# Kernel tuning notes

Measured on AMD Instinct MI355X. Metric: run time of the kernel, lower is better.

The kernel has to match this reference:

```python
import jax, jax.numpy as jnp
import numpy as np

N_LEVELS = 16
F = 2
LOG2_T = 19
T = 1 << LOG2_T
BASE_RES = 16.0
FINEST_RES = 512.0
N_SAMPLES = 128
NEAR, FAR = 2.0, 6.0
BOX_MIN = jnp.array([-1.5, -1.5, -1.5], jnp.float32)
BOX_MAX = jnp.array([1.5, 1.5, 1.5], jnp.float32)
GEO_FEAT = 15
OUT_CH = 4

_PRIMES = np.array([1, 2654435761, 805459861], dtype=np.uint32)
_OFFSETS = np.array([[i, j, k] for i in (0, 1) for j in (0, 1) for k in (0, 1)], dtype=np.int32)  # [8,3]
_B = np.exp((np.log(FINEST_RES) - np.log(BASE_RES)) / (N_LEVELS - 1))
_RESOLUTIONS = np.floor(BASE_RES * _B ** np.arange(N_LEVELS)).astype(np.float32)


def setup_inputs() -> dict:
    key = jax.random.key(0)
    ks = jax.random.split(key, 10)
    n_rays = 16384
    o = jax.random.uniform(ks[0], (n_rays, 3), jnp.float32, -0.5, 0.5)
    d = jax.random.normal(ks[1], (n_rays, 3), jnp.float32)
    d = d / jnp.linalg.norm(d, axis=-1, keepdims=True)
    rays = jnp.concatenate([o, d], -1)
    hash_tables = jax.random.uniform(ks[2], (N_LEVELS, T, F), jnp.float32, -1e-4, 1e-4)
    def w(k, di, do):
        return jax.random.normal(k, (di, do), jnp.float32) * (1.0 / np.sqrt(di))
    return dict(
        rays=rays,
        hash_tables=hash_tables,
        ws0=w(ks[3], 32, 64), ws1=w(ks[4], 64, 64), ws2=w(ks[5], 64, 1 + GEO_FEAT),
        wc0=w(ks[6], 16 + GEO_FEAT, 64), wc1=w(ks[7], 64, 64), wc2=w(ks[8], 64, 64), wc3=w(ks[9], 64, OUT_CH - 1),
    )


def _hash_embed(x, tables):
    """Multi-res hash grid: x [P,3] world coords, tables [L,T,F] -> ([P,L*F], keep_mask [P])."""
    xc = jnp.clip(x, BOX_MIN, BOX_MAX)
    keep = jnp.all(x == xc, axis=-1)
    offs = jnp.asarray(_OFFSETS)          # [8,3]
    primes = jnp.asarray(_PRIMES)         # uint32
    feats = []
    for l in range(N_LEVELS):
        grid = (BOX_MAX - BOX_MIN) / _RESOLUTIONS[l]
        bl = jnp.floor((xc - BOX_MIN) / grid).astype(jnp.int32)   # [P,3] bottom-left voxel index
        vmin = bl.astype(jnp.float32) * grid + BOX_MIN
        wts = (xc - vmin) / grid                                  # trilinear weights [P,3]
        corners = (bl[:, None, :] + offs[None]).astype(jnp.uint32)  # [P,8,3]
        h = (corners[..., 0] * primes[0]) ^ (corners[..., 1] * primes[1]) ^ (corners[..., 2] * primes[2])
        idx = (h & jnp.uint32(T - 1)).astype(jnp.int32)           # [P,8]
        e = tables[l][idx]                                        # [P,8,F]
        w0, w1, w2 = wts[:, 0:1], wts[:, 1:2], wts[:, 2:3]
        c00 = e[:, 0] * (1 - w0) + e[:, 4] * w0
        c01 = e[:, 1] * (1 - w0) + e[:, 5] * w0
        c10 = e[:, 2] * (1 - w0) + e[:, 6] * w0
        c11 = e[:, 3] * (1 - w0) + e[:, 7] * w0
        c0 = c00 * (1 - w1) + c10 * w1
        c1 = c01 * (1 - w1) + c11 * w1
        feats.append(c0 * (1 - w2) + c1 * w2)
    return jnp.concatenate(feats, -1), keep


def _sh_encode(d):
    """Degree-4 spherical harmonics encoding, [P,3] -> [P,16]."""
    x, y, z = d[..., 0], d[..., 1], d[..., 2]
    xx, yy, zz = x * x, y * y, z * z
    xy, yz, xz = x * y, y * z, x * z
    C0 = 0.28209479177387814
    C1 = 0.4886025119029199
    C2 = (1.0925484305920792, -1.0925484305920792, 0.31539156525252005, -1.0925484305920792, 0.5462742152960396)
    C3 = (-0.5900435899266435, 2.890611442640554, -0.4570457994644658, 0.3731763325901154,
          -0.4570457994644658, 1.445305721320277, -0.5900435899266435)
    return jnp.stack([
        jnp.full_like(x, C0),
        -C1 * y, C1 * z, -C1 * x,
        C2[0] * xy, C2[1] * yz, C2[2] * (2.0 * zz - xx - yy), C2[3] * xz, C2[4] * (xx - yy),
        C3[0] * y * (3.0 * xx - yy), C3[1] * xy * z, C3[2] * y * (4.0 * zz - xx - yy),
        C3[3] * z * (2.0 * zz - 3.0 * xx - 3.0 * yy), C3[4] * x * (4.0 * zz - xx - yy),
        C3[5] * z * (xx - yy), C3[6] * x * (xx - 3.0 * yy),
    ], axis=-1)


def _forward(rays, hash_tables, ws0, ws1, ws2, wc0, wc1, wc2, wc3):
    n_rays = rays.shape[0]
    o, d = rays[:, :3], rays[:, 3:6]
    z = jnp.linspace(NEAR, FAR, N_SAMPLES, dtype=jnp.float32)
    zvals = jnp.broadcast_to(z, (n_rays, N_SAMPLES))
    pts = o[:, None, :] + d[:, None, :] * z[None, :, None]       # [N,S,3]
    P = n_rays * N_SAMPLES
    pts_f = pts.reshape(P, 3)
    dirs_f = jnp.broadcast_to(d[:, None, :], (n_rays, N_SAMPLES, 3)).reshape(P, 3)

    enc_pts, keep = _hash_embed(pts_f, hash_tables)              # [P,32], [P]
    enc_dirs = _sh_encode(dirs_f)                                # [P,16]

    # NeRFSmall: bias-free sigma net then color net
    h = jnp.maximum(enc_pts @ ws0, 0.0)
    h = jnp.maximum(h @ ws1, 0.0)
    h = h @ ws2                                                   # [P, 1+GEO_FEAT]
    sigma, geo = h[:, 0], h[:, 1:]
    hc = jnp.concatenate([enc_dirs, geo], -1)
    hc = jnp.maximum(hc @ wc0, 0.0)
    hc = jnp.maximum(hc @ wc1, 0.0)
    hc = jnp.maximum(hc @ wc2, 0.0)
    color = hc @ wc3                                              # [P, OUT_CH-1]

    sigma = jnp.where(keep, sigma, 0.0)                           # output[~keep_mask, -1] = 0
    raw = jnp.concatenate([color, sigma[:, None]], -1).reshape(n_rays, N_SAMPLES, OUT_CH)

    # Integrator (raw2outputs)
    dists = zvals[:, 1:] - zvals[:, :-1]
    dists = jnp.concatenate([dists, jnp.full((n_rays, 1), 1e10, jnp.float32)], -1)
    dists = dists * jnp.linalg.norm(d, axis=-1, keepdims=True)
    chs = jax.nn.sigmoid(raw[..., :-1])
    alpha = 1.0 - jnp.exp(-jnp.maximum(raw[..., -1], 0.0) * dists)
    trans = jnp.cumprod(1.0 - alpha + 1e-10, axis=-1)
    trans = jnp.concatenate([jnp.ones((n_rays, 1), jnp.float32), trans[:, :-1]], -1)
    weights = alpha * trans
    chs_map = jnp.einsum('ns,nsc->nc', weights, chs)
    depth_map = jnp.sum(weights * zvals, -1)
    probs = jnp.concatenate([weights, 1.0 - jnp.sum(weights, -1, keepdims=True) + 1e-6], -1)
    p = probs / jnp.sum(probs, -1, keepdims=True)
    sparsity_loss = -jnp.sum(p * jnp.log(jnp.clip(p, 1e-37)), -1)
    return chs_map, depth_map, sparsity_loss


def reference(rays, hash_tables, ws0, ws1, ws2, wc0, wc1, wc2, wc3):
    return _forward(rays, hash_tables, ws0, ws1, ws2, wc0, wc1, wc2, wc3)
```

## Files before the change

### kernel.cpp

```cpp
#include <hip/hip_runtime.h>

#define NRAYS 16384
#define NLEV  16
#define THASH 524288
#define MAXACT 48
#define MAXPTS (NRAYS*MAXACT)
#define MBLK  512
#define MGRID 1024

__device__ __forceinline__ float zval32(int i) {
  const float step = 4.0f / 127.0f;
  return __fadd_rn(2.0f, __fmul_rn((float)i, step));
}
__device__ __forceinline__ float pcoord(float o, float d, float z) {
  return __fadd_rn(o, __fmul_rn(d, z));
}

__global__ __launch_bounds__(64)
void k_classify(const float* __restrict__ rays,
                float* __restrict__ sh,
                unsigned* __restrict__ rn) {
  int r = blockIdx.x * 64 + threadIdx.x;
  if (r >= NRAYS) return;
  float ox = rays[6*r+0], oy = rays[6*r+1], oz = rays[6*r+2];
  float dx = rays[6*r+3], dy = rays[6*r+4], dz = rays[6*r+5];
  float x = dx, y = dy, z = dz;
  float xx = x*x, yy = y*y, zz = z*z, xy = x*y, yz = y*z, xz = x*z;
  float* shp = sh + 16*r;
  shp[0]  = 0.28209479177387814f;
  shp[1]  = -0.4886025119029199f * y;
  shp[2]  =  0.4886025119029199f * z;
  shp[3]  = -0.4886025119029199f * x;
  shp[4]  =  1.0925484305920792f * xy;
  shp[5]  = -1.0925484305920792f * yz;
  shp[6]  =  0.31539156525252005f * (2.0f*zz - xx - yy);
  shp[7]  = -1.0925484305920792f * xz;
  shp[8]  =  0.5462742152960396f * (xx - yy);
  shp[9]  = -0.5900435899266435f * y * (3.0f*xx - yy);
  shp[10] =  2.890611442640554f  * xy * z;
  shp[11] = -0.4570457994644658f * y * (4.0f*zz - xx - yy);
  shp[12] =  0.3731763325901154f * z * (2.0f*zz - 3.0f*xx - 3.0f*yy);
  shp[13] = -0.4570457994644658f * x * (4.0f*zz - xx - yy);
  shp[14] =  1.445305721320277f  * z * (xx - yy);
  shp[15] = -0.5900435899266435f * x * (xx - 3.0f*yy);
  int n = 0;
  for (int i = 0; i < 128; ++i) {
    float zi = zval32(i);
    float px = pcoord(ox, dx, zi);
    float py = pcoord(oy, dy, zi);
    float pz = pcoord(oz, dz, zi);
    bool in = (px >= -1.5f) && (px <= 1.5f) && (py >= -1.5f) && (py <= 1.5f)
           && (pz >= -1.5f) && (pz <= 1.5f);
    if (!in) break;
    ++n;
  }
  rn[r] = (unsigned)n;
}

__global__ __launch_bounds__(1024)
void k_scan(const unsigned* __restrict__ rn,
            unsigned* __restrict__ rbase,
            unsigned* __restrict__ counter,
            unsigned* __restrict__ plist) {
  __shared__ unsigned wsum[16];
  const int t = threadIdx.x;
  const int lane = t & 63, wid = t >> 6;
  unsigned nv[16];
  const uint4* rn4 = (const uint4*)rn;
  unsigned tot = 0;
#pragma unroll
  for (int k = 0; k < 4; ++k) {
    uint4 a = rn4[t*4 + k];
    nv[4*k+0] = a.x; nv[4*k+1] = a.y; nv[4*k+2] = a.z; nv[4*k+3] = a.w;
    tot += a.x + a.y + a.z + a.w;
  }
  unsigned incl = tot;
#pragma unroll
  for (int off = 1; off < 64; off <<= 1) {
    unsigned v = __shfl_up(incl, off);
    if (lane >= off) incl += v;
  }
  if (lane == 63) wsum[wid] = incl;
  __syncthreads();
  if (t == 0) {
    unsigned acc = 0;
#pragma unroll
    for (int w = 0; w < 16; ++w) { unsigned x = wsum[w]; wsum[w] = acc; acc += x; }
    *counter = acc;
  }
  __syncthreads();
  unsigned base = wsum[wid] + (incl - tot);
#pragma unroll
  for (int j = 0; j < 16; ++j) {
    int r = t*16 + j;
    rbase[r] = base;
    unsigned nj = nv[j];
    for (unsigned i = 0; i < nj; ++i) plist[base + i] = (unsigned)(r*128) + i;
    base += nj;
  }
}

template<int IN, int TOTOUT, int JC, bool RELU>
__device__ __forceinline__ void layer(const float* __restrict__ W, int jbase,
                                      const float* __restrict__ in,
                                      float* __restrict__ out, int lane) {
  float acc[JC];
#pragma unroll
  for (int j = 0; j < JC; ++j) acc[j] = 0.0f;
#pragma unroll 4
  for (int k = 0; k < IN; ++k) {
    float a = in[k*64 + lane];
    const float* Wk = W + k*TOTOUT + jbase;
#pragma unroll
    for (int j = 0; j < JC; ++j) acc[j] = fmaf(a, Wk[j], acc[j]);
  }
#pragma unroll
  for (int j = 0; j < JC; ++j)
    out[(jbase + j)*64 + lane] = RELU ? fmaxf(acc[j], 0.0f) : acc[j];
}

__global__ __launch_bounds__(MBLK)
void k_mlp(const float* __restrict__ rays,
           const float* __restrict__ tables,
           const float* __restrict__ w_s0, const float* __restrict__ w_s1,
           const float* __restrict__ w_s2, const float* __restrict__ w_c0,
           const float* __restrict__ w_c1, const float* __restrict__ w_c2,
           const float* __restrict__ w_c3,
           const float* __restrict__ sh,
           const unsigned* __restrict__ counter,
           const unsigned* __restrict__ plist,
           float4* __restrict__ results) {
  __shared__ float bufA[64*64];
  __shared__ float bufB[64*64];
  __shared__ float sig_s[64];
  __shared__ unsigned pid_s[64];
  const int t = threadIdx.x;
  const int lane = t & 63;
  const int q = __builtin_amdgcn_readfirstlane(t >> 6);
  const unsigned count = *counter;
  const unsigned ntiles = (count + 63u) >> 6;
  const float RESF[NLEV] = {16.f,20.f,25.f,32.f,40.f,50.f,64.f,80.f,
                            101.f,128.f,161.f,203.f,256.f,322.f,406.f,512.f};
  for (unsigned tile = blockIdx.x; tile < ntiles; tile += MGRID) {
    unsigned s0 = tile << 6;
    if (t < 64) {
      unsigned s = s0 + (unsigned)t;
      pid_s[t] = (s < count) ? plist[s] : 0u;
    }
    __syncthreads();
    {
      unsigned pid = pid_s[lane];
      int r = (int)(pid >> 7);
      int i = (int)(pid & 127u);
      float zi = zval32(i);
      float px = pcoord(rays[6*r+0], rays[6*r+3], zi);
      float py = pcoord(rays[6*r+1], rays[6*r+4], zi);
      float pz = pcoord(rays[6*r+2], rays[6*r+5], zi);
      float xcx = fminf(fmaxf(px, -1.5f), 1.5f);
      float xcy = fminf(fmaxf(py, -1.5f), 1.5f);
      float xcz = fminf(fmaxf(pz, -1.5f), 1.5f);
#pragma unroll
      for (int li = 0; li < 2; ++li) {
        int l = 2*q + li;
        const float grid = 3.0f / RESF[l];
        float bfx = floorf(__fdiv_rn(__fadd_rn(xcx, 1.5f), grid));
        float bfy = floorf(__fdiv_rn(__fadd_rn(xcy, 1.5f), grid));
        float bfz = floorf(__fdiv_rn(__fadd_rn(xcz, 1.5f), grid));
        float vmx = __fadd_rn(__fmul_rn(bfx, grid), -1.5f);
        float vmy = __fadd_rn(__fmul_rn(bfy, grid), -1.5f);
        float vmz = __fadd_rn(__fmul_rn(bfz, grid), -1.5f);
        float wx = __fdiv_rn(__fsub_rn(xcx, vmx), grid);
        float wy = __fdiv_rn(__fsub_rn(xcy, vmy), grid);
        float wz = __fdiv_rn(__fsub_rn(xcz, vmz), grid);
        unsigned cx0 = (unsigned)(int)bfx, cy0 = (unsigned)(int)bfy, cz0 = (unsigned)(int)bfz;
        unsigned cx1 = cx0 + 1u, cy1 = cy0 + 1u, cz1 = cz0 + 1u;
        unsigned hy0 = cy0*2654435761u, hy1 = cy1*2654435761u;
        unsigned hz0 = cz0*805459861u,  hz1 = cz1*805459861u;
        const float2* tb = (const float2*)tables + (size_t)l*THASH;
        float2 e000 = tb[(cx0^hy0^hz0)&(THASH-1)];
        float2 e001 = tb[(cx0^hy0^hz1)&(THASH-1)];
        float2 e010 = tb[(cx0^hy1^hz0)&(THASH-1)];
        float2 e011 = tb[(cx0^hy1^hz1)&(THASH-1)];
        float2 e100 = tb[(cx1^hy0^hz0)&(THASH-1)];
        float2 e101 = tb[(cx1^hy0^hz1)&(THASH-1)];
        float2 e110 = tb[(cx1^hy1^hz0)&(THASH-1)];
        float2 e111 = tb[(cx1^hy1^hz1)&(THASH-1)];
        float iwx = 1.f-wx, iwy = 1.f-wy, iwz = 1.f-wz;
        float c00a = e000.x*iwx + e100.x*wx, c00b = e000.y*iwx + e100.y*wx;
        float c01a = e001.x*iwx + e101.x*wx, c01b = e001.y*iwx + e101.y*wx;
        float c10a = e010.x*iwx + e110.x*wx, c10b = e010.y*iwx + e110.y*wx;
        float c11a = e011.x*iwx + e111.x*wx, c11b = e011.y*iwx + e111.y*wx;
        float c0a = c00a*iwy + c10a*wy, c0b = c00b*iwy + c10b*wy;
        float c1a = c01a*iwy + c11a*wy, c1b = c01b*iwy + c11b*wy;
        bufA[(2*l+0)*64 + lane] = c0a*iwz + c1a*wz;
        bufA[(2*l+1)*64 + lane] = c0b*iwz + c1b*wz;
      }
    }
    __syncthreads();
    layer<32,64,8,true >(w_s0, q*8, bufA, bufB, lane); __syncthreads();
    layer<64,64,8,true >(w_s1, q*8, bufB, bufA, lane); __syncthreads();
    layer<64,16,2,false>(w_s2, q*2, bufA, bufB, lane); __syncthreads();
    if (q == 0) sig_s[lane] = bufB[0*64 + lane];
    for (int idx = t; idx < 31*64; idx += MBLK) {
      int k = idx >> 6, p = idx & 63;
      float v;
      if (k < 16) v = sh[(pid_s[p] >> 7)*16 + k];
      else        v = bufB[(k-15)*64 + p];
      bufA[idx] = v;
    }
    __syncthreads();
    layer<31,64,8,true >(w_c0, q*8, bufA, bufB, lane); __syncthreads();
    layer<64,64,8,true >(w_c1, q*8, bufB, bufA, lane); __syncthreads();
    layer<64,64,8,true >(w_c2, q*8, bufA, bufB, lane); __syncthreads();
    if (q < 3) layer<64,3,1,false>(w_c3, q, bufB, bufA, lane);
    __syncthreads();
    if (q == 0) {
      unsigned s = s0 + (unsigned)lane;
      if (s < count) {
        float4 res;
        res.x = sig_s[lane];
        res.y = bufA[0*64 + lane];
        res.z = bufA[1*64 + lane];
        res.w = bufA[2*64 + lane];
        results[s] = res;
      }
    }
    __syncthreads();
  }
}

__global__ __launch_bounds__(256)
void k_comp(const float* __restrict__ rays,
            const unsigned* __restrict__ rbase,
            const unsigned* __restrict__ rn,
            const float4* __restrict__ results,
            float* __restrict__ out) {
  __shared__ float s_al[4][64];
  __shared__ float s_c0[4][64];
  __shared__ float s_c1[4][64];
  __shared__ float s_c2[4][64];
  const int wid  = threadIdx.x >> 6;
  const int lane = threadIdx.x & 63;
  const int r = blockIdx.x * 4 + wid;
  float dx = rays[6*r+3], dy = rays[6*r+4], dz = rays[6*r+5];
  float dnorm = sqrtf(dx*dx + dy*dy + dz*dz);
  const int n = (int)rn[r];
  const unsigned base = rbase[r];
  const float step = 4.0f/127.0f;
  const float diststep = __fmul_rn(step, dnorm);
  if (lane < n) {
    float4 rs = results[base + lane];
    float sg = fmaxf(rs.x, 0.f);
    s_al[wid][lane] = -expm1f(-__fmul_rn(sg, diststep));
    s_c0[wid][lane] = 1.f/(1.f + expf(-rs.y));
    s_c1[wid][lane] = 1.f/(1.f + expf(-rs.z));
    s_c2[wid][lane] = 1.f/(1.f + expf(-rs.w));
  }
  __syncthreads();
  if (lane == 0) {
    float S = 0.f, ch0 = 0.f, ch1 = 0.f, ch2 = 0.f, dep = 0.f, trans = 1.f;
    for (int i = 0; i < n; ++i) {
      float alpha = s_al[wid][i];
      float w = __fmul_rn(alpha, trans);
      trans = __fmul_rn(trans, __fadd_rn(__fsub_rn(1.f, alpha), 1e-10f));
      S += w; ch0 += w*s_c0[wid][i]; ch1 += w*s_c1[wid][i]; ch2 += w*s_c2[wid][i];
      dep += w*zval32(i);
    }
    float rem  = __fadd_rn(__fsub_rn(1.f, S), 1e-6f);
    float Stot = __fadd_rn(S, rem);
    float loss = 0.f, trans2 = 1.f;
    for (int i = 0; i < n; ++i) {
      float alpha = s_al[wid][i];
      float w = __fmul_rn(alpha, trans2);
      trans2 = __fmul_rn(trans2, __fadd_rn(__fsub_rn(1.f, alpha), 1e-10f));
      float p = __fdiv_rn(w, Stot);
      loss += p * logf(fmaxf(p, 1e-37f));
    }
    float pl = __fdiv_rn(rem, Stot);
    loss += pl * logf(fmaxf(pl, 1e-37f));
    out[3*r+0] = ch0; out[3*r+1] = ch1; out[3*r+2] = ch2;
    out[3*NRAYS + r] = dep;
    out[4*NRAYS + r] = -loss;
  }
}

extern "C" void kernel_launch(void* const* d_in, const int* in_sizes, int n_in,
                              void* d_out, int out_size, void* d_ws, size_t ws_size,
                              hipStream_t stream) {
  const float* rays   = (const float*)d_in[0];
  const float* tables = (const float*)d_in[1];
  const float* ws0    = (const float*)d_in[2];
  const float* ws1    = (const float*)d_in[3];
  const float* ws2    = (const float*)d_in[4];
  const float* wc0    = (const float*)d_in[5];
  const float* wc1    = (const float*)d_in[6];
  const float* wc2    = (const float*)d_in[7];
  const float* wc3    = (const float*)d_in[8];

  char* ws = (char*)d_ws;
  unsigned* counter = (unsigned*)ws;
  unsigned* rbase   = (unsigned*)(ws + 256);
  unsigned* rn      = (unsigned*)(ws + 256 + 65536);
  float*    sh      = (float*)  (ws + 256 + 131072);
  float4*   results = (float4*) (ws + 1179904);
  unsigned* plist   = (unsigned*)(ws + 1179904 + (size_t)MAXPTS*16);

  k_classify<<<NRAYS/64, 64, 0, stream>>>(rays, sh, rn);
  k_scan<<<1, 1024, 0, stream>>>(rn, rbase, counter, plist);
  k_mlp<<<MGRID, MBLK, 0, stream>>>(rays, tables, ws0, ws1, ws2,
                                    wc0, wc1, wc2, wc3, sh, counter, plist, results);
  k_comp<<<NRAYS/4, 256, 0, stream>>>(rays, rbase, rn, results, (float*)d_out);
}
```

Measured before the change: 206.7 us.

## Rewrite compositing as one thread per ray, prefetch MLP weights, unroll layer loop more

The compositing kernel now gives each ray its own thread and walks that ray's samples serially. The old version used one wave per ray with a shared-memory stage and a single-lane scan. The new loops recompute alpha in the second pass and read results directly with strided per-thread float4 loads. The MLP kernel warms the weight matrices into cache at start by touching one float per 16 bytes. The layer k-loop unroll goes from 4 to 8. Tradeoffs: per-thread gathers in compositing are uncoalesced, the extra prefetch loads run in every block, and the larger unroll raises register pressure.

```diff
diff --git a/kernel.cpp b/kernel.cpp
--- a/kernel.cpp
+++ b/kernel.cpp
@@ -107,7 +107,7 @@
   float acc[JC];
 #pragma unroll
   for (int j = 0; j < JC; ++j) acc[j] = 0.0f;
-#pragma unroll 4
+#pragma unroll 8
   for (int k = 0; k < IN; ++k) {
     float a = in[k*64 + lane];
     const float* Wk = W + k*TOTOUT + jbase;
@@ -137,6 +137,18 @@
   const int t = threadIdx.x;
   const int lane = t & 63;
   const int q = __builtin_amdgcn_readfirstlane(t >> 6);
+  {
+    float pf = 0.f;
+    const float4* a;
+    a = (const float4*)w_s0; for (int i = t; i < 512;  i += MBLK) pf += a[i].x;
+    a = (const float4*)w_s1; for (int i = t; i < 1024; i += MBLK) pf += a[i].x;
+    a = (const float4*)w_s2; for (int i = t; i < 256;  i += MBLK) pf += a[i].x;
+    a = (const float4*)w_c0; for (int i = t; i < 496;  i += MBLK) pf += a[i].x;
+    a = (const float4*)w_c1; for (int i = t; i < 1024; i += MBLK) pf += a[i].x;
+    a = (const float4*)w_c2; for (int i = t; i < 1024; i += MBLK) pf += a[i].x;
+    a = (const float4*)w_c3; for (int i = t; i < 48;   i += MBLK) pf += a[i].x;
+    asm volatile("" :: "v"(pf));
+  }
   const unsigned count = *counter;
   const unsigned ntiles = (count + 63u) >> 6;
   const float RESF[NLEV] = {16.f,20.f,25.f,32.f,40.f,50.f,64.f,80.f,
@@ -229,59 +241,50 @@
   }
 }
 
-__global__ __launch_bounds__(256)
+__global__ __launch_bounds__(64)
 void k_comp(const float* __restrict__ rays,
             const unsigned* __restrict__ rbase,
             const unsigned* __restrict__ rn,
             const float4* __restrict__ results,
             float* __restrict__ out) {
-  __shared__ float s_al[4][64];
-  __shared__ float s_c0[4][64];
-  __shared__ float s_c1[4][64];
-  __shared__ float s_c2[4][64];
-  const int wid  = threadIdx.x >> 6;
-  const int lane = threadIdx.x & 63;
-  const int r = blockIdx.x * 4 + wid;
+  int r = blockIdx.x * 64 + threadIdx.x;
+  if (r >= NRAYS) return;
   float dx = rays[6*r+3], dy = rays[6*r+4], dz = rays[6*r+5];
   float dnorm = sqrtf(dx*dx + dy*dy + dz*dz);
-  const int n = (int)rn[r];
-  const unsigned base = rbase[r];
+  int n = (int)rn[r];
+  unsigned base = rbase[r];
   const float step = 4.0f/127.0f;
   const float diststep = __fmul_rn(step, dnorm);
-  if (lane < n) {
-    float4 rs = results[base + lane];
+  float S = 0.f, ch0 = 0.f, ch1 = 0.f, ch2 = 0.f, dep = 0.f, trans = 1.f;
+  for (int i = 0; i < n; ++i) {
+    float4 rs = results[base + i];
+    float z = zval32(i);
     float sg = fmaxf(rs.x, 0.f);
-    s_al[wid][lane] = -expm1f(-__fmul_rn(sg, diststep));
-    s_c0[wid][lane] = 1.f/(1.f + expf(-rs.y));
-    s_c1[wid][lane] = 1.f/(1.f + expf(-rs.z));
-    s_c2[wid][lane] = 1.f/(1.f + expf(-rs.w));
-  }
-  __syncthreads();
-  if (lane == 0) {
-    float S = 0.f, ch0 = 0.f, ch1 = 0.f, ch2 = 0.f, dep = 0.f, trans = 1.f;
-    for (int i = 0; i < n; ++i) {
-      float alpha = s_al[wid][i];
-      float w = __fmul_rn(alpha, trans);
-      trans = __fmul_rn(trans, __fadd_rn(__fsub_rn(1.f, alpha), 1e-10f));
-      S += w; ch0 += w*s_c0[wid][i]; ch1 += w*s_c1[wid][i]; ch2 += w*s_c2[wid][i];
-      dep += w*zval32(i);
-    }
-    float rem  = __fadd_rn(__fsub_rn(1.f, S), 1e-6f);
-    float Stot = __fadd_rn(S, rem);
-    float loss = 0.f, trans2 = 1.f;
-    for (int i = 0; i < n; ++i) {
-      float alpha = s_al[wid][i];
-      float w = __fmul_rn(alpha, trans2);
-      trans2 = __fmul_rn(trans2, __fadd_rn(__fsub_rn(1.f, alpha), 1e-10f));
-      float p = __fdiv_rn(w, Stot);
-      loss += p * logf(fmaxf(p, 1e-37f));
-    }
-    float pl = __fdiv_rn(rem, Stot);
-    loss += pl * logf(fmaxf(pl, 1e-37f));
-    out[3*r+0] = ch0; out[3*r+1] = ch1; out[3*r+2] = ch2;
-    out[3*NRAYS + r] = dep;
-    out[4*NRAYS + r] = -loss;
-  }
+    float alpha = -expm1f(-__fmul_rn(sg, diststep));
+    float w = __fmul_rn(alpha, trans);
+    trans = __fmul_rn(trans, __fadd_rn(__fsub_rn(1.f, alpha), 1e-10f));
+    float s0 = 1.f/(1.f + expf(-rs.y));
+    float s1 = 1.f/(1.f + expf(-rs.z));
+    float s2 = 1.f/(1.f + expf(-rs.w));
+    S += w; ch0 += w*s0; ch1 += w*s1; ch2 += w*s2; dep += w*z;
+  }
+  float rem  = __fadd_rn(__fsub_rn(1.f, S), 1e-6f);
+  float Stot = __fadd_rn(S, rem);
+  float loss = 0.f, trans2 = 1.f;
+  for (int i = 0; i < n; ++i) {
+    float4 rs = results[base + i];
+    float sg = fmaxf(rs.x, 0.f);
+    float alpha = -expm1f(-__fmul_rn(sg, diststep));
+    float w = __fmul_rn(alpha, trans2);
+    trans2 = __fmul_rn(trans2, __fadd_rn(__fsub_rn(1.f, alpha), 1e-10f));
+    float p = __fdiv_rn(w, Stot);
+    loss += p * logf(fmaxf(p, 1e-37f));
+  }
+  float pl = __fdiv_rn(rem, Stot);
+  loss += pl * logf(fmaxf(pl, 1e-37f));
+  out[3*r+0] = ch0; out[3*r+1] = ch1; out[3*r+2] = ch2;
+  out[3*NRAYS + r] = dep;
+  out[4*NRAYS + r] = -loss;
 }
 
 extern "C" void kernel_launch(void* const* d_in, const int* in_sizes, int n_in,
@@ -309,5 +312,5 @@
   k_scan<<<1, 1024, 0, stream>>>(rn, rbase, counter, plist);
   k_mlp<<<MGRID, MBLK, 0, stream>>>(rays, tables, ws0, ws1, ws2,
                                     wc0, wc1, wc2, wc3, sh, counter, plist, results);
-  k_comp<<<NRAYS/4, 256, 0, stream>>>(rays, rbase, rn, results, (float*)d_out);
-}
+  k_comp<<<NRAYS/64, 64, 0, stream>>>(rays, rbase, rn, results, (float*)d_out);
+}
```

Result: slower. 216.0 us (+4.5%).
